# Kernel optimization log

Measured on AMD Instinct MI355X. Metric: run time of the kernel, lower is better.

## Reference

```python
import math
import jax, jax.numpy as jnp
import numpy as np

B, L, H, E = 2, 4096, 8, 64          # q/k/v input layout [B, L, H, E], H*E = embed_dim = 512
NUM_HEADS = 4                        # num_heads // 2
HEAD_DIM = 64                        # embed_dim // NUM_HEADS // 2
LAMBDA_INIT = 0.8 - 0.6 * math.exp(-0.3 * 0)  # depth = 0 -> 0.2


def setup_inputs() -> dict:
    key = jax.random.key(0)
    ks = jax.random.split(key, 8)
    q = jax.random.normal(ks[0], (B, L, H, E), jnp.float32)
    k = jax.random.normal(ks[1], (B, L, H, E), jnp.float32)
    v = jax.random.normal(ks[2], (B, L, H, E), jnp.float32)
    attn_mask = jnp.zeros((L, L), jnp.float32)
    lambda_q1 = 0.1 * jax.random.normal(ks[3], (HEAD_DIM,), jnp.float32)
    lambda_k1 = 0.1 * jax.random.normal(ks[4], (HEAD_DIM,), jnp.float32)
    lambda_q2 = 0.1 * jax.random.normal(ks[5], (HEAD_DIM,), jnp.float32)
    lambda_k2 = 0.1 * jax.random.normal(ks[6], (HEAD_DIM,), jnp.float32)
    return {"q": q, "k": k, "v": v, "attn_mask": attn_mask,
            "lambda_q1": lambda_q1, "lambda_k1": lambda_k1,
            "lambda_q2": lambda_q2, "lambda_k2": lambda_k2}


def reference(q, k, v, attn_mask, lambda_q1, lambda_k1, lambda_q2, lambda_k2):
    Bq, Lq, Hq, Eq = q.shape
    scaling = HEAD_DIM ** (-0.5)
    # split each attention head into two differential sub-heads
    qh = q.reshape(Bq, Lq, 2 * NUM_HEADS, HEAD_DIM).transpose(0, 2, 1, 3) * scaling  # [B,2h,L,d]
    kh = k.reshape(Bq, Lq, 2 * NUM_HEADS, HEAD_DIM).transpose(0, 2, 1, 3)            # [B,2h,L,d]
    vh = v.reshape(Bq, Lq, NUM_HEADS, 2 * HEAD_DIM).transpose(0, 2, 1, 3)            # [B,h,L,2d]

    scores = jnp.einsum('bhld,bhsd->bhls', qh, kh)  # [B,2h,L,L]
    scores = jnp.nan_to_num(scores) + attn_mask
    probs = jax.nn.softmax(scores, axis=-1)

    lam1 = jnp.exp(jnp.sum(lambda_q1 * lambda_k1))
    lam2 = jnp.exp(jnp.sum(lambda_q2 * lambda_k2))
    lam_full = lam1 - lam2 + LAMBDA_INIT

    probs = probs.reshape(Bq, NUM_HEADS, 2, Lq, Lq)
    w = probs[:, :, 0] - lam_full * probs[:, :, 1]          # [B,h,L,L]
    out = jnp.einsum('bhls,bhsd->bhld', w, vh)              # [B,h,L,2d]
    out = out * (1.0 - LAMBDA_INIT)
    return out.transpose(0, 2, 1, 3).reshape(Bq, Lq, Hq, Eq)
```

## Files before the change

### kernel.cpp

```cpp
#include <hip/hip_runtime.h>
#include <hip/hip_bf16.h>


typedef __attribute__((ext_vector_type(8))) short s16x8;
typedef __attribute__((ext_vector_type(16))) float f32x16;
typedef __attribute__((ext_vector_type(4))) unsigned int u32x4;

#define MFMA32(a,b,c) __builtin_amdgcn_mfma_f32_32x32x16_bf16(a,b,c,0,0,0)
#define GLD16(gp, lp) __builtin_amdgcn_global_load_lds( \
    (__attribute__((address_space(1))) void*)(gp), \
    (__attribute__((address_space(3))) void*)(lp), 16, 0, 0)

__device__ __forceinline__ unsigned pk2(float a, float b){
  union { __hip_bfloat162 h; unsigned u; } cv;
  cv.h = __float22bfloat162_rn(float2{a, b});
  return cv.u;
}

__global__ void k_prep_qk(const float* __restrict__ q, const float* __restrict__ k,
                          char* __restrict__ qfr, char* __restrict__ kfr){
  int idx = blockIdx.x*256 + threadIdx.x;
  int j8 = idx & 7;
  int l  = (idx >> 3) & 4095;
  int h  = (idx >> 15) & 7;
  int b  = idx >> 18;
  size_t src = ((size_t)(b*4096 + l))*512 + h*64 + j8*8;
  const float* qp = q + src;
  const float* kp = k + src;
  const float s = 0.125f * 1.4426950408889634f;
  u32x4 qw, kw;
  #pragma unroll
  for (int i=0;i<4;i++){
    qw[i] = pk2(qp[2*i]*s, qp[2*i+1]*s);
    kw[i] = pk2(kp[2*i],   kp[2*i+1]);
  }
  int dstep = j8 >> 1, hi = j8 & 1;
  int lane16 = (l & 31) + 32*hi;
  size_t qdst = ((((size_t)(b*8+h)*128 + (l>>5))*4 + dstep) << 10) + (size_t)lane16*16;
  size_t kdst = ((((size_t)(b*8+h)*64 + (l>>6))*8 + ((l>>5)&1)*4 + dstep) << 10) + (size_t)lane16*16;
  *(u32x4*)(qfr + qdst) = qw;
  *(u32x4*)(kfr + kdst) = kw;
}

__global__ void k_prep_v(const float* __restrict__ v, char* __restrict__ vfr,
                         const float* __restrict__ lq1, const float* __restrict__ lk1,
                         const float* __restrict__ lq2, const float* __restrict__ lk2,
                         float* __restrict__ lam_out){
  if (blockIdx.x == 0 && threadIdx.x < 64){
    int l = threadIdx.x;
    float p1 = lq1[l]*lk1[l];
    float p2 = lq2[l]*lk2[l];
    #pragma unroll
    for (int m=1;m<64;m<<=1){ p1 += __shfl_xor(p1,m,64); p2 += __shfl_xor(p2,m,64); }
    if (l==0) lam_out[0] = expf(p1) - expf(p2) + 0.2f;
  }
  __shared__ float tl[64][132];
  int bid = blockIdx.x;
  int tile = bid & 63, hp = (bid>>6)&3, b = bid>>8;
  int t = threadIdx.x;
  #pragma unroll
  for (int i=0;i<32;i++){
    int idx = t + i*256;
    int s = idx >> 7, e = idx & 127;
    tl[s][e] = v[((size_t)(b*4096 + tile*64 + s))*512 + hp*128 + e];
  }
  __syncthreads();
  size_t base = ((size_t)((b*4+hp)*64 + tile))*16384;
  #pragma unroll
  for (int i=0;i<4;i++){
    int idx = t + i*256;
    int g = idx >> 6, l = idx & 63;
    int eb = g >> 2, ss = g & 3;
    int e = eb*32 + (l & 31);
    int s0 = ss*16 + (l>>5)*8;
    u32x4 w;
    #pragma unroll
    for (int jj=0;jj<4;jj++) w[jj] = pk2(tl[s0+2*jj][e], tl[s0+2*jj+1][e]);
    *(u32x4*)(vfr + base + g*1024 + l*16) = w;
  }
}

__device__ __forceinline__ void swap32(unsigned a, unsigned bv, int lane,
                                       unsigned &r0, unsigned &r1){
#if __has_builtin(__builtin_amdgcn_permlane32_swap)
  auto pr = __builtin_amdgcn_permlane32_swap(a, bv, false, false);
  r0 = pr[0]; r1 = pr[1];
#else
  unsigned ax = (unsigned)__shfl_xor((int)a, 32, 64);
  unsigned bx = (unsigned)__shfl_xor((int)bv, 32, 64);
  bool lo = lane < 32;
  r0 = lo ? a  : bx;
  r1 = lo ? ax : bv;
#endif
}
__device__ __forceinline__ s16x8 mkfrag2(const f32x16& p, int base, int lane){
  unsigned A0 = pk2(p[base+0],p[base+1]), A1 = pk2(p[base+2],p[base+3]);
  unsigned B0 = pk2(p[base+4],p[base+5]), B1 = pk2(p[base+6],p[base+7]);
  unsigned w0,w1,w2,w3;
  swap32(A0,B0,lane,w0,w2);
  swap32(A1,B1,lane,w1,w3);
  union { unsigned u[4]; s16x8 v; } r;
  r.u[0]=w0; r.u[1]=w1; r.u[2]=w2; r.u[3]=w3;
  return r.v;
}

__launch_bounds__(256, 2)
__global__ void k_attn(const char* __restrict__ qfrag, const char* __restrict__ kfrag,
                       const char* __restrict__ vfrag, const float* __restrict__ lamp,
                       float* __restrict__ out){
  __shared__ __align__(16) char lds[65536];
  int tid = threadIdx.x, lane = tid & 63, wave = tid >> 6;
  int bid = blockIdx.x;
  int y = bid & 7, qt = bid >> 3;
  int b = y >> 2, hp = y & 3;
  int sh = wave & 1, qh = wave >> 1;
  int lq = lane & 31, hi = lane >> 5;

  s16x8 qf[4];
  {
    const char* qp = qfrag + ((((size_t)(b*8 + 2*hp + sh)*128 + (qt*2 + qh))*4) << 10);
    #pragma unroll
    for (int d=0; d<4; d++) qf[d] = *(const s16x8*)(qp + d*1024 + lane*16);
  }
  const f32x16 Z = {0.f,0.f,0.f,0.f,0.f,0.f,0.f,0.f,0.f,0.f,0.f,0.f,0.f,0.f,0.f,0.f};
  f32x16 o[4];
  #pragma unroll
  for (int eb=0; eb<4; eb++) o[eb] = Z;
  float den = 0.f;

  const char* gK = kfrag + ((size_t)(b*8 + 2*hp))*64*8192;
  const char* gV = vfrag + ((size_t)(b*4 + hp))*64*16384;
  const char* sg; int sld; size_t sstride;
  if      (wave==0){ sg = gK;          sld = 0;     sstride = 8192; }
  else if (wave==1){ sg = gK + (size_t)64*8192; sld = 8192;  sstride = 8192; }
  else if (wave==2){ sg = gV;          sld = 16384; sstride = 16384; }
  else             { sg = gV + 8192;   sld = 24576; sstride = 16384; }

#define STAGE(BUFB, TT) { const char* src_ = sg + (size_t)(TT)*sstride; \
    char* dst_ = (char*)lds + (BUFB) + sld; \
    _Pragma("unroll") \
    for (int i_=0;i_<8;i_++) GLD16(src_ + i_*1024 + lane*16, dst_ + i_*1024); }

  STAGE(0, 0)
  __syncthreads();
  int cur = 0;

  for (int t=0; t<64; t++){
    if (t < 63) STAGE((cur^1)*32768, t+1)

    const char* Bb = lds + cur*32768;
    const char* Kb = Bb + sh*8192;
    const char* Vb = Bb + 16384;

    f32x16 sA, sB;
    {
      s16x8 ka0 = *(const s16x8*)(Kb +        lane*16);
      s16x8 kb0 = *(const s16x8*)(Kb + 4096 + lane*16);
      __builtin_amdgcn_s_setprio(1);
      sA = MFMA32(ka0, qf[0], Z);
      sB = MFMA32(kb0, qf[0], Z);
      __builtin_amdgcn_s_setprio(0);
      #pragma unroll
      for (int d=1; d<4; d++){
        s16x8 ka = *(const s16x8*)(Kb + d*1024 +        lane*16);
        s16x8 kb = *(const s16x8*)(Kb + d*1024 + 4096 + lane*16);
        __builtin_amdgcn_s_setprio(1);
        sA = MFMA32(ka, qf[d], sA);
        sB = MFMA32(kb, qf[d], sB);
        __builtin_amdgcn_s_setprio(0);
      }
    }

    #pragma unroll
    for (int i=0;i<16;i++){
      sA[i] = __builtin_amdgcn_exp2f(sA[i]);
      sB[i] = __builtin_amdgcn_exp2f(sB[i]);
    }
    float c0 = sA[0]+sB[0], c1 = sA[1]+sB[1], c2 = sA[2]+sB[2], c3 = sA[3]+sB[3];
    #pragma unroll
    for (int i=4; i<16; i+=4){
      c0 += sA[i]   + sB[i];
      c1 += sA[i+1] + sB[i+1];
      c2 += sA[i+2] + sB[i+2];
      c3 += sA[i+3] + sB[i+3];
    }
    float rs = (c0+c1) + (c2+c3);
    den += rs + __shfl_xor(rs, 32, 64);

    s16x8 pf[4];
    pf[0] = mkfrag2(sA, 0, lane);
    pf[1] = mkfrag2(sA, 8, lane);
    pf[2] = mkfrag2(sB, 0, lane);
    pf[3] = mkfrag2(sB, 8, lane);

    #pragma unroll
    for (int ss=0; ss<4; ss++){
      #pragma unroll
      for (int eb=0; eb<4; eb++){
        s16x8 vf = *(const s16x8*)(Vb + (eb*4+ss)*1024 + lane*16);
        __builtin_amdgcn_s_setprio(1);
        o[eb] = MFMA32(vf, pf[ss], o[eb]);
        __builtin_amdgcn_s_setprio(0);
      }
    }

    __syncthreads();
    cur ^= 1;
  }

  float invl = 1.0f / den;
  float lam = lamp[0];
  float* xb = (float*)lds;
  if (sh){
    float sc1 = lam * invl;
    float* dst = xb + qh*4224 + lq*132;
    #pragma unroll
    for (int eb=0;eb<4;eb++){
      #pragma unroll
      for (int tq=0;tq<4;tq++){
        int e = eb*32 + 8*tq + 4*hi;
        float4 w;
        w.x = o[eb][4*tq+0]*sc1; w.y = o[eb][4*tq+1]*sc1;
        w.z = o[eb][4*tq+2]*sc1; w.w = o[eb][4*tq+3]*sc1;
        *(float4*)(dst + e) = w;
      }
    }
  }
  __syncthreads();
  if (!sh){
    const float* srcp = xb + qh*4224 + lq*132;
    int qrow = qt*64 + qh*32 + lq;
    float* op = out + ((size_t)(b*4096 + qrow))*512 + hp*128;
    #pragma unroll
    for (int eb=0;eb<4;eb++){
      #pragma unroll
      for (int tq=0;tq<4;tq++){
        int e = eb*32 + 8*tq + 4*hi;
        float4 w1 = *(const float4*)(srcp + e);
        float4 r;
        r.x = 0.8f*(o[eb][4*tq+0]*invl - w1.x);
        r.y = 0.8f*(o[eb][4*tq+1]*invl - w1.y);
        r.z = 0.8f*(o[eb][4*tq+2]*invl - w1.z);
        r.w = 0.8f*(o[eb][4*tq+3]*invl - w1.w);
        *(float4*)(op + e) = r;
      }
    }
  }
#undef STAGE
}

extern "C" void kernel_launch(void* const* d_in, const int* in_sizes, int n_in,
                              void* d_out, int out_size, void* d_ws, size_t ws_size,
                              hipStream_t stream){
  const float* q   = (const float*)d_in[0];
  const float* k   = (const float*)d_in[1];
  const float* v   = (const float*)d_in[2];
  const float* lq1 = (const float*)d_in[4];
  const float* lk1 = (const float*)d_in[5];
  const float* lq2 = (const float*)d_in[6];
  const float* lk2 = (const float*)d_in[7];
  float* out = (float*)d_out;

  char* ws = (char*)d_ws;
  char* qfr = ws;
  char* kfr = ws + 8388608;
  char* vfr = ws + 16777216;
  float* lam = (float*)(ws + 25165824);

  k_prep_qk<<<2048, 256, 0, stream>>>(q, k, qfr, kfr);
  k_prep_v <<<512,  256, 0, stream>>>(v, vfr, lq1, lk1, lq2, lk2, lam);
  k_attn   <<<512,  256, 0, stream>>>(qfr, kfr, vfr, lam, out);
}
```

Before: 142.7 us.

## Software-pipeline QK softmax of next tile ahead of PV MMA

New measurement: 136.7 us. 4.2% less time.

```diff
diff --git a/kernel.cpp b/kernel.cpp
--- a/kernel.cpp
+++ b/kernel.cpp
@@ -141,73 +141,79 @@
     _Pragma("unroll") \
     for (int i_=0;i_<8;i_++) GLD16(src_ + i_*1024 + lane*16, dst_ + i_*1024); }
 
+#define QKSM(SLOTB) { \
+    const char* Kb_ = lds + (SLOTB) + sh*8192; \
+    f32x16 sA, sB; \
+    { \
+      s16x8 ka0 = *(const s16x8*)(Kb_ +        lane*16); \
+      s16x8 kb0 = *(const s16x8*)(Kb_ + 4096 + lane*16); \
+      __builtin_amdgcn_s_setprio(1); \
+      sA = MFMA32(ka0, qf[0], Z); \
+      sB = MFMA32(kb0, qf[0], Z); \
+      __builtin_amdgcn_s_setprio(0); \
+      _Pragma("unroll") \
+      for (int d=1; d<4; d++){ \
+        s16x8 ka = *(const s16x8*)(Kb_ + d*1024 +        lane*16); \
+        s16x8 kb = *(const s16x8*)(Kb_ + d*1024 + 4096 + lane*16); \
+        __builtin_amdgcn_s_setprio(1); \
+        sA = MFMA32(ka, qf[d], sA); \
+        sB = MFMA32(kb, qf[d], sB); \
+        __builtin_amdgcn_s_setprio(0); \
+      } \
+    } \
+    _Pragma("unroll") \
+    for (int i=0;i<16;i++){ \
+      sA[i] = __builtin_amdgcn_exp2f(sA[i]); \
+      sB[i] = __builtin_amdgcn_exp2f(sB[i]); \
+    } \
+    float c0 = sA[0]+sB[0], c1 = sA[1]+sB[1], c2 = sA[2]+sB[2], c3 = sA[3]+sB[3]; \
+    _Pragma("unroll") \
+    for (int i=4; i<16; i+=4){ \
+      c0 += sA[i]   + sB[i]; \
+      c1 += sA[i+1] + sB[i+1]; \
+      c2 += sA[i+2] + sB[i+2]; \
+      c3 += sA[i+3] + sB[i+3]; \
+    } \
+    den += (c0+c1) + (c2+c3); \
+    pf[0] = mkfrag2(sA, 0, lane); \
+    pf[1] = mkfrag2(sA, 8, lane); \
+    pf[2] = mkfrag2(sB, 0, lane); \
+    pf[3] = mkfrag2(sB, 8, lane); \
+  }
+
+  s16x8 pf[4];
+
   STAGE(0, 0)
   __syncthreads();
+  QKSM(0)
   int cur = 0;
 
   for (int t=0; t<64; t++){
     if (t < 63) STAGE((cur^1)*32768, t+1)
 
-    const char* Bb = lds + cur*32768;
-    const char* Kb = Bb + sh*8192;
-    const char* Vb = Bb + 16384;
-
-    f32x16 sA, sB;
     {
-      s16x8 ka0 = *(const s16x8*)(Kb +        lane*16);
-      s16x8 kb0 = *(const s16x8*)(Kb + 4096 + lane*16);
-      __builtin_amdgcn_s_setprio(1);
-      sA = MFMA32(ka0, qf[0], Z);
-      sB = MFMA32(kb0, qf[0], Z);
-      __builtin_amdgcn_s_setprio(0);
+      const char* Vb = lds + cur*32768 + 16384;
       #pragma unroll
-      for (int d=1; d<4; d++){
-        s16x8 ka = *(const s16x8*)(Kb + d*1024 +        lane*16);
-        s16x8 kb = *(const s16x8*)(Kb + d*1024 + 4096 + lane*16);
-        __builtin_amdgcn_s_setprio(1);
-        sA = MFMA32(ka, qf[d], sA);
-        sB = MFMA32(kb, qf[d], sB);
-        __builtin_amdgcn_s_setprio(0);
+      for (int ss=0; ss<4; ss++){
+        #pragma unroll
+        for (int eb=0; eb<4; eb++){
+          s16x8 vf = *(const s16x8*)(Vb + (eb*4+ss)*1024 + lane*16);
+          __builtin_amdgcn_s_setprio(1);
+          o[eb] = MFMA32(vf, pf[ss], o[eb]);
+          __builtin_amdgcn_s_setprio(0);
+        }
       }
     }
 
-    #pragma unroll
-    for (int i=0;i<16;i++){
-      sA[i] = __builtin_amdgcn_exp2f(sA[i]);
-      sB[i] = __builtin_amdgcn_exp2f(sB[i]);
-    }
-    float c0 = sA[0]+sB[0], c1 = sA[1]+sB[1], c2 = sA[2]+sB[2], c3 = sA[3]+sB[3];
-    #pragma unroll
-    for (int i=4; i<16; i+=4){
-      c0 += sA[i]   + sB[i];
-      c1 += sA[i+1] + sB[i+1];
-      c2 += sA[i+2] + sB[i+2];
-      c3 += sA[i+3] + sB[i+3];
-    }
-    float rs = (c0+c1) + (c2+c3);
-    den += rs + __shfl_xor(rs, 32, 64);
-
-    s16x8 pf[4];
-    pf[0] = mkfrag2(sA, 0, lane);
-    pf[1] = mkfrag2(sA, 8, lane);
-    pf[2] = mkfrag2(sB, 0, lane);
-    pf[3] = mkfrag2(sB, 8, lane);
-
-    #pragma unroll
-    for (int ss=0; ss<4; ss++){
-      #pragma unroll
-      for (int eb=0; eb<4; eb++){
-        s16x8 vf = *(const s16x8*)(Vb + (eb*4+ss)*1024 + lane*16);
-        __builtin_amdgcn_s_setprio(1);
-        o[eb] = MFMA32(vf, pf[ss], o[eb]);
-        __builtin_amdgcn_s_setprio(0);
-      }
-    }
-
-    __syncthreads();
-    cur ^= 1;
-  }
-
+    if (t < 63){
+      __syncthreads();
+      QKSM((cur^1)*32768)
+      cur ^= 1;
+    }
+  }
+  den += __shfl_xor(den, 32, 64);
+
+  __syncthreads();
   float invl = 1.0f / den;
   float lam = lamp[0];
   float* xb = (float*)lds;
@@ -247,6 +253,7 @@
     }
   }
 #undef STAGE
+#undef QKSM
 }
 
 extern "C" void kernel_launch(void* const* d_in, const int* in_sizes, int n_in,
```
